# Performance work log

Hardware: AMD Instinct MI355X
Metric: run time of the kernel (lower is better)

The kernel has to match this reference:

```python
import jax, jax.numpy as jnp
import numpy as np

B, T, C, HS = 4, 2048, 1024, 16
H = C // HS
LAYER_ID, N_LAYER = 2, 24
D_MIX, D_DECAY = 32, 64
LN_EPS = 1e-5


def setup_inputs() -> dict:
    key = jax.random.key(0)
    ks = jax.random.split(key, 8)
    r01 = LAYER_ID / (N_LAYER - 1)
    r10 = 1.0 - LAYER_ID / N_LAYER
    ddd = (np.arange(C, dtype=np.float64) / C)
    tm = lambda p: (1.0 - ddd ** p).reshape(1, 1, C).astype(np.float32)
    time_maa_x = tm(r10)
    time_maa_w = tm(r10)
    time_maa_k = tm(r10)
    time_maa_v = (1.0 - (ddd ** r10 + 0.3 * r01)).reshape(1, 1, C).astype(np.float32)
    time_maa_r = tm(0.5 * r10)
    n = np.arange(C, dtype=np.float64)
    decay = (-6.0 + 5.0 * (n / (C - 1)) ** (0.7 + 1.3 * r01)).reshape(1, 1, C).astype(np.float32)
    zig = ((n + 1) % 3 - 1) * 0.1
    faaaa = (r01 * (1.0 - n / (C - 1)) + zig).reshape(H, HS).astype(np.float32)
    u01 = lambda k, s: jax.random.uniform(k, s, jnp.float32, -0.01, 0.01)
    return {
        "x": jax.random.normal(ks[0], (B, T, C), jnp.float32),
        "time_maa_x": jnp.asarray(time_maa_x),
        "time_maa_w": jnp.asarray(time_maa_w),
        "time_maa_k": jnp.asarray(time_maa_k),
        "time_maa_v": jnp.asarray(time_maa_v),
        "time_maa_r": jnp.asarray(time_maa_r),
        "time_maa_w1": u01(ks[1], (C, D_MIX * 4)),
        "time_maa_w2": u01(ks[2], (4, D_MIX, C)),
        "time_decay": jnp.asarray(decay),
        "time_decay_w1": u01(ks[3], (C, D_DECAY)),
        "time_decay_w2": u01(ks[4], (D_DECAY, C)),
        "time_faaaa": jnp.asarray(faaaa),
        "W_r": jax.random.normal(ks[5], (C, C), jnp.float32) * 0.02,
        "W_k": jax.random.normal(ks[6], (C, C), jnp.float32) * 0.02,
        "W_v": jax.random.normal(ks[7], (C, C), jnp.float32) * 0.02,
        "W_o": jax.random.normal(jax.random.fold_in(key, 99), (C, C), jnp.float32) * 0.02,
        "ln_g": jnp.ones((C,), jnp.float32),
        "ln_b": jnp.zeros((C,), jnp.float32),
    }


def _wkv6(r, k, v, w, u):
    # r,k,v,w: [B,T,H,N]; u: [H,N]. Per-head 16x16 state, rank-1 updates.
    wd = jnp.exp(-jnp.exp(w))  # decay in (0,1)
    rT, kT, vT, wT = (a.transpose(1, 0, 2, 3) for a in (r, k, v, wd))  # [T,B,H,N]

    def step(S, ins):
        r_t, k_t, v_t, w_t = ins  # each [B,H,N]
        kv = jnp.einsum("bhi,bhj->bhij", k_t, v_t)
        y_t = jnp.einsum("bhi,bhij->bhj", r_t, S + u[None, :, :, None] * kv)
        return w_t[..., None] * S + kv, y_t

    S0 = jnp.zeros((r.shape[0], H, HS, HS), r.dtype)
    _, ys = jax.lax.scan(step, S0, (rT, kT, vT, wT))  # ys: [T,B,H,N]
    return ys.transpose(1, 0, 2, 3)


def reference(x, time_maa_x, time_maa_w, time_maa_k, time_maa_v, time_maa_r,
              time_maa_w1, time_maa_w2, time_decay, time_decay_w1, time_decay_w2,
              time_faaaa, W_r, W_k, W_v, W_o, ln_g, ln_b):
    b, t, c = x.shape
    # time shift: previous token (zero at t=0)
    xx = jnp.concatenate([jnp.zeros_like(x[:, :1]), x[:, :-1]], axis=1) - x
    xxx = x + xx * time_maa_x
    m = jnp.tanh(xxx @ time_maa_w1).reshape(b, t, 4, D_MIX)
    m = jnp.einsum("btfd,fdc->fbtc", m, time_maa_w2)  # [4,B,T,C]
    mw, mk, mv, mr = m[0], m[1], m[2], m[3]
    xw = x + xx * (time_maa_w + mw)
    xk = x + xx * (time_maa_k + mk)
    xv = x + xx * (time_maa_v + mv)
    xr = x + xx * (time_maa_r + mr)
    r = (xr @ W_r).reshape(b, t, H, HS)
    k = (xk @ W_k).reshape(b, t, H, HS)
    v = (xv @ W_v).reshape(b, t, H, HS)
    ww = jnp.tanh(xw @ time_decay_w1) @ time_decay_w2
    w = (time_decay + ww).reshape(b, t, H, HS)
    y = _wkv6(r, k, v, w, time_faaaa).reshape(b, t, c)
    mu = jnp.mean(y, axis=-1, keepdims=True)
    var = jnp.mean(jnp.square(y - mu), axis=-1, keepdims=True)
    y = (y - mu) * jax.lax.rsqrt(var + LN_EPS) * ln_g + ln_b
    return y @ W_o
```

## Files before the change

### kernel.cpp

```cpp
#include <hip/hip_runtime.h>
#include <stdint.h>

#define TT 2048
#define CC 1024

typedef short bf16x8 __attribute__((ext_vector_type(8)));
typedef float f32x4 __attribute__((ext_vector_type(4)));
typedef unsigned uint2v __attribute__((ext_vector_type(2)));
typedef __attribute__((address_space(3))) uint32_t lds_u32_t;
typedef const __attribute__((address_space(1))) uint32_t glb_u32_t;

__device__ inline unsigned short f2b(float f) {
  union { float f; unsigned u; } c; c.f = f;
  unsigned u = c.u;
  return (unsigned short)((u + 0x7fffu + ((u >> 16) & 1u)) >> 16);
}
__device__ inline float b2f(unsigned short s) {
  union { unsigned u; float f; } c; c.u = ((unsigned)s) << 16; return c.f;
}

__device__ inline void gl_lds16(const void* g, void* l) {
  glb_u32_t* gp = (glb_u32_t*)(uintptr_t)g;
  lds_u32_t* lp = (lds_u32_t*)(uint32_t)(uintptr_t)l;
  __builtin_amdgcn_global_load_lds(gp, lp, 16, 0, 0);
}

__device__ inline void swiz(int& bx, int& by, int& bz) {
  int nx = gridDim.x, ny = gridDim.y;
  int flat = (blockIdx.z * ny + blockIdx.y) * nx + blockIdx.x;
  int xcd = flat & 7;
  int idx = flat >> 3;
  int perz = (nx * ny) >> 3;
  bz = idx / perz;
  int rem = idx - bz * perz;
  int r = rem / nx;
  bx = rem - r * nx;
  by = xcd * (ny >> 3) + r;
}

struct TSeg { const float* in; unsigned short* out; int R, C, tx, start; };
struct TransAll { TSeg seg[11]; int nseg; };
__global__ void transpose_all(TransAll ta) {
  __shared__ float tile[32][33];
  int bid = blockIdx.x;
  int si = 0;
  while (si + 1 < ta.nseg && bid >= ta.seg[si + 1].start) si++;
  TSeg sg = ta.seg[si];
  int lt = bid - sg.start;
  int bx = lt % sg.tx, by = lt / sg.tx;
  int c0 = bx * 32, r0 = by * 32;
  int tx = threadIdx.x, ty = threadIdx.y;
  for (int i = ty; i < 32; i += 8) {
    int r = r0 + i, c = c0 + tx;
    tile[i][tx] = (r < sg.R && c < sg.C) ? sg.in[(size_t)r * sg.C + c] : 0.f;
  }
  __syncthreads();
  int rr = r0 + tx;
  for (int i = ty; i < 32; i += 8) {
    int cc = c0 + i;
    if (cc < sg.C && rr < sg.R) sg.out[(size_t)cc * sg.R + rr] = f2b(tile[tx][i]);
  }
}

__global__ void shift_mix(const float* __restrict__ x, const float* __restrict__ tmx,
                          unsigned short* __restrict__ xb, unsigned short* __restrict__ xxb,
                          unsigned short* __restrict__ xxx) {
  int idx = blockIdx.x * 256 + threadIdx.x;
  int c4 = idx & 255;
  int row = idx >> 8;
  int t = row & (TT - 1);
  const float4* x4 = (const float4*)x;
  float4 xv = x4[idx];
  float4 pv = make_float4(0.f, 0.f, 0.f, 0.f);
  if (t > 0) pv = x4[idx - 256];
  float4 d;
  d.x = pv.x - xv.x; d.y = pv.y - xv.y; d.z = pv.z - xv.z; d.w = pv.w - xv.w;
  ushort4 ob;
  ob.x = f2b(xv.x); ob.y = f2b(xv.y); ob.z = f2b(xv.z); ob.w = f2b(xv.w);
  ((ushort4*)xb)[idx] = ob;
  ushort4 od;
  od.x = f2b(d.x); od.y = f2b(d.y); od.z = f2b(d.z); od.w = f2b(d.w);
  ((ushort4*)xxb)[idx] = od;
  float4 tm = ((const float4*)tmx)[c4];
  ushort4 o;
  o.x = f2b(xv.x + d.x * tm.x);
  o.y = f2b(xv.y + d.y * tm.y);
  o.z = f2b(xv.z + d.z * tm.z);
  o.w = f2b(xv.w + d.w * tm.w);
  ((ushort4*)xxx)[idx] = o;
}

__device__ __forceinline__ void gemm_core_pipe(
    const unsigned short* __restrict__ A, const unsigned short* __restrict__ Bt,
    int k0beg, int k0end, int lda, int ldb, int rowBase, int colBase,
    unsigned short* As, unsigned short* Bs, f32x4 acc[4][4], int w, int lane,
    int quad, int l16, int waveM, int waveN) {
#pragma unroll
  for (int i = 0; i < 4; i++)
#pragma unroll
    for (int j = 0; j < 4; j++) acc[i][j] = (f32x4){0.f, 0.f, 0.f, 0.f};
  const int SSB = 8192;
  const int nIter = (k0end - k0beg) >> 5;
  int rl = lane >> 2;
  int cl = (lane & 3) ^ ((lane >> 3) & 3);
  int rA0 = w * 16 + rl, rA1 = (w + 4) * 16 + rl;
  const unsigned short* gA0 = A + (size_t)(rowBase + rA0) * lda + cl * 8 + k0beg;
  const unsigned short* gA1 = A + (size_t)(rowBase + rA1) * lda + cl * 8 + k0beg;
  const unsigned short* gB0 = Bt + (size_t)(colBase + rA0) * ldb + cl * 8 + k0beg;
  const unsigned short* gB1 = Bt + (size_t)(colBase + rA1) * ldb + cl * 8 + k0beg;
  char* dA0 = (char*)As + w * 1024;
  char* dA1 = (char*)As + (w + 4) * 1024;
  char* dB0 = (char*)Bs + w * 1024;
  char* dB1 = (char*)Bs + (w + 4) * 1024;
  int sw = quad ^ ((l16 >> 1) & 3);
  int aoff = (waveM + l16) * 64 + sw * 16;
  int boff = (waveN + l16) * 64 + sw * 16;

#define ISSUE(it, st)                               \
  {                                                 \
    int ko = (it) * 32;                             \
    gl_lds16(gA0 + ko, dA0 + (st) * SSB);           \
    gl_lds16(gA1 + ko, dA1 + (st) * SSB);           \
    gl_lds16(gB0 + ko, dB0 + (st) * SSB);           \
    gl_lds16(gB1 + ko, dB1 + (st) * SSB);           \
  }

  ISSUE(0, 0)
  if (nIter > 1) ISSUE(1, 1)
  int stage = 0;
  for (int it = 0; it < nIter; ++it) {
    if (it + 1 < nIter) {
      asm volatile("s_waitcnt vmcnt(4)\ns_barrier" ::: "memory");
    } else {
      asm volatile("s_waitcnt vmcnt(0)\ns_barrier" ::: "memory");
    }
    if (it + 2 < nIter) {
      int ns = stage + 2; if (ns >= 3) ns -= 3;
      ISSUE(it + 2, ns)
    }
    const char* Ab = (const char*)As + stage * SSB;
    const char* Bb = (const char*)Bs + stage * SSB;
    bf16x8 af[4], bfr[4];
#pragma unroll
    for (int mt = 0; mt < 4; mt++)
      af[mt] = *(const bf16x8*)(Ab + aoff + mt * 1024);
#pragma unroll
    for (int nt = 0; nt < 4; nt++)
      bfr[nt] = *(const bf16x8*)(Bb + boff + nt * 1024);
#pragma unroll
    for (int mt = 0; mt < 4; mt++)
#pragma unroll
      for (int nt = 0; nt < 4; nt++)
        acc[mt][nt] = __builtin_amdgcn_mfma_f32_16x16x32_bf16(af[mt], bfr[nt], acc[mt][nt], 0, 0, 0);
    stage = stage + 1; if (stage >= 3) stage -= 3;
  }
#undef ISSUE
}

__global__ __launch_bounds__(256) void gemm_bf16(
    const unsigned short* __restrict__ A, const unsigned short* __restrict__ Bt,
    int N, int K, int lda, int ldb, int mode, int ldc,
    float* __restrict__ outF, unsigned short* __restrict__ outB,
    const float* __restrict__ tm) {
  __shared__ __align__(16) unsigned short As[3 * 4096];
  __shared__ __align__(16) unsigned short Bs[3 * 4096];
  int bx, by, bz;
  swiz(bx, by, bz);
  (void)bz;
  int tid = threadIdx.x;
  int w = tid >> 6, lane = tid & 63;
  int quad = lane >> 4, l16 = lane & 15;
  int rowBase = by * 128;
  int colBase = bx * 128;
  int waveM = (w >> 1) * 64, waveN = (w & 1) * 64;
  f32x4 acc[4][4];
  gemm_core_pipe(A, Bt, 0, K, lda, ldb, rowBase, colBase, As, Bs, acc, w, lane, quad, l16, waveM, waveN);
#pragma unroll
  for (int mt = 0; mt < 4; mt++)
#pragma unroll
    for (int nt = 0; nt < 4; nt++)
#pragma unroll
      for (int rg = 0; rg < 4; rg++) {
        int row = rowBase + waveM + mt * 16 + quad * 4 + rg;
        int col = colBase + waveN + nt * 16 + l16;
        if (col >= N) continue;
        float val = acc[mt][nt][rg];
        if (mode == 0) {
          outF[(size_t)row * ldc + col] = val;
        } else {
          int b = row >> 11, t = row & (TT - 1), h = col >> 4, n = col & 15;
          outF[(size_t)((b * 64 + h) * TT + t) * 16 + n] = expf(-expf(tm[col] + val));
        }
      }
}

__global__ __launch_bounds__(256) void gemm_splitk(
    const unsigned short* __restrict__ A, const unsigned short* __restrict__ Bt,
    int N, int Kc, int lda, int ldb, int ldp, float* __restrict__ part) {
  __shared__ __align__(16) unsigned short As[3 * 4096];
  __shared__ __align__(16) unsigned short Bs[3 * 4096];
  int s = blockIdx.x, by = blockIdx.y;
  int M = gridDim.y * 128;
  int tid = threadIdx.x;
  int w = tid >> 6, lane = tid & 63;
  int quad = lane >> 4, l16 = lane & 15;
  int rowBase = by * 128;
  int waveM = (w >> 1) * 64, waveN = (w & 1) * 64;
  f32x4 acc[4][4];
  gemm_core_pipe(A, Bt, s * Kc, (s + 1) * Kc, lda, ldb, rowBase, 0, As, Bs, acc, w, lane, quad, l16, waveM, waveN);
  float* pb = part + (size_t)s * M * ldp;
#pragma unroll
  for (int mt = 0; mt < 4; mt++)
#pragma unroll
    for (int nt = 0; nt < 4; nt++)
#pragma unroll
      for (int rg = 0; rg < 4; rg++) {
        int row = rowBase + waveM + mt * 16 + quad * 4 + rg;
        int col = waveN + nt * 16 + l16;
        if (col < N) pb[(size_t)row * ldp + col] = acc[mt][nt][rg];
      }
}

__global__ __launch_bounds__(256) void reduce_tanh(
    const float* __restrict__ part, unsigned short* __restrict__ out,
    int total4, int S, int strideElems) {
  int idx = blockIdx.x * 256 + threadIdx.x;
  if (idx >= total4) return;
  float4 a = ((const float4*)part)[idx];
  for (int s = 1; s < S; s++) {
    float4 b = ((const float4*)(part + (size_t)s * strideElems))[idx];
    a.x += b.x; a.y += b.y; a.z += b.z; a.w += b.w;
  }
  ushort4 o;
  o.x = f2b(tanhf(a.x)); o.y = f2b(tanhf(a.y));
  o.z = f2b(tanhf(a.z)); o.w = f2b(tanhf(a.w));
  ((ushort4*)out)[idx] = o;
}

struct GateArgs {
  const unsigned short* A;
  const unsigned short* Bt;
  unsigned short* out[4];
  const float* tm[4];
  const unsigned short* xb;
  const unsigned short* xxb;
};
__global__ __launch_bounds__(256) void gemm_gate4(GateArgs ga) {
  __shared__ __align__(16) unsigned short As[3 * 4096];
  __shared__ __align__(16) unsigned short Bs[3 * 4096];
  int flat = (blockIdx.z * 64 + blockIdx.y) * 8 + blockIdx.x;
  int xcd = flat & 7;
  int idx = flat >> 3;
  int z = idx & 3;
  int tile = idx >> 2;
  int by = xcd * 8 + (tile >> 3);
  int bx = tile & 7;
  const unsigned short* A = ga.A + z * 32;
  const unsigned short* Bt = ga.Bt + (size_t)z * 1024 * 32;
  unsigned short* outB = ga.out[z];
  const float* tm = ga.tm[z];
  int tid = threadIdx.x;
  int w = tid >> 6, lane = tid & 63;
  int quad = lane >> 4, l16 = lane & 15;
  int rowBase = by * 128;
  int colBase = bx * 128;
  int waveM = (w >> 1) * 64, waveN = (w & 1) * 64;
  f32x4 acc[4][4];
  gemm_core_pipe(A, Bt, 0, 32, 128, 32, rowBase, colBase, As, Bs, acc, w, lane, quad, l16, waveM, waveN);
#pragma unroll
  for (int mt = 0; mt < 4; mt++)
#pragma unroll
    for (int nt = 0; nt < 4; nt++)
#pragma unroll
      for (int rg = 0; rg < 4; rg++) {
        int row = rowBase + waveM + mt * 16 + quad * 4 + rg;
        int col = colBase + waveN + nt * 16 + l16;
        size_t o = (size_t)row * CC + col;
        float xv = b2f(ga.xb[o]), xxv = b2f(ga.xxb[o]);
        outB[o] = f2b(xv + xxv * (tm[col] + acc[mt][nt][rg]));
      }
}

struct ProjArgs {
  const unsigned short* A[3];
  const unsigned short* Bt[3];
  unsigned short* out[3];
};
__global__ __launch_bounds__(256) void gemm_proj3(ProjArgs pa) {
  __shared__ __align__(16) unsigned short As[3 * 4096];
  __shared__ __align__(16) unsigned short Bs[3 * 4096];
  int bx, by, bz;
  swiz(bx, by, bz);
  const unsigned short* A = pa.A[bz];
  const unsigned short* Bt = pa.Bt[bz];
  unsigned short* outB = pa.out[bz];
  int tid = threadIdx.x;
  int w = tid >> 6, lane = tid & 63;
  int quad = lane >> 4, l16 = lane & 15;
  int rowBase = by * 128;
  int colBase = bx * 128;
  int waveM = (w >> 1) * 64, waveN = (w & 1) * 64;
  f32x4 acc[4][4];
  gemm_core_pipe(A, Bt, 0, 1024, 1024, 1024, rowBase, colBase, As, Bs, acc, w, lane, quad, l16, waveM, waveN);
#pragma unroll
  for (int mt = 0; mt < 4; mt++)
#pragma unroll
    for (int nt = 0; nt < 4; nt++)
#pragma unroll
      for (int rg = 0; rg < 4; rg++) {
        int row = rowBase + waveM + mt * 16 + quad * 4 + rg;
        int col = colBase + waveN + nt * 16 + l16;
        int b = row >> 11, t = row & (TT - 1), h = col >> 4, n = col & 15;
        outB[(size_t)((b * 64 + h) * TT + t) * 16 + n] = f2b(acc[mt][nt][rg]);
      }
}

__device__ __forceinline__ float reduce_p(float part) {
#if __has_builtin(__builtin_amdgcn_permlane32_swap) && __has_builtin(__builtin_amdgcn_permlane16_swap)
  uint2v a = __builtin_amdgcn_permlane32_swap(__float_as_uint(part), __float_as_uint(part), false, false);
  float s1 = part + __uint_as_float(a.y);
  uint2v b = __builtin_amdgcn_permlane16_swap(__float_as_uint(s1), __float_as_uint(s1), false, false);
  return s1 + __uint_as_float(b.y);
#else
  part += __shfl_xor(part, 16, 64);
  part += __shfl_xor(part, 32, 64);
  return part;
#endif
}

__global__ __launch_bounds__(1024) void wkv_scan2(
    const unsigned short* __restrict__ r, const unsigned short* __restrict__ k,
    const unsigned short* __restrict__ v, const float* __restrict__ wd,
    const float* __restrict__ u, float* __restrict__ y) {
  __shared__ __align__(16) unsigned short lrb[16][256];
  __shared__ __align__(16) unsigned short lkb[16][256];
  __shared__ __align__(16) unsigned short lvb[16][256];
  __shared__ __align__(16) float lw[16][256];
  __shared__ __align__(16) float Lend[16][256];
  __shared__ __align__(16) float Sini[16][256];
  __shared__ float Eend[16][16];
  int bh = blockIdx.x;
  int b = bh >> 6, h = bh & 63;
  int tid = threadIdx.x;
  int c = tid >> 6, lane = tid & 63;
  int j = lane & 15, p = lane >> 4;
  size_t base = (size_t)bh * TT * 16 + (size_t)c * 128 * 16;

  float S0 = 0.f, S1 = 0.f, S2 = 0.f, S3 = 0.f;
  float E0 = 1.f, E1 = 1.f, E2 = 1.f, E3 = 1.f;
  for (int t0 = 0; t0 < 128; t0 += 16) {
    size_t off = base + (size_t)t0 * 16;
    ushort4 kv4 = ((const ushort4*)(k + off))[lane];
    ushort4 vv = ((const ushort4*)(v + off))[lane];
    float4 wv = ((const float4*)(wd + off))[lane];
    ((ushort4*)lkb[c])[lane] = kv4;
    ((ushort4*)lvb[c])[lane] = vv;
    ((float4*)lw[c])[lane] = wv;
#pragma unroll
    for (int s = 0; s < 16; s++) {
      ushort4 kk = *(const ushort4*)(lkb[c] + s * 16 + p * 4);
      float4 ww = *(const float4*)(lw[c] + s * 16 + p * 4);
      float vj = b2f(lvb[c][s * 16 + j]);
      S0 = fmaf(ww.x, S0, b2f(kk.x) * vj); E0 *= ww.x;
      S1 = fmaf(ww.y, S1, b2f(kk.y) * vj); E1 *= ww.y;
      S2 = fmaf(ww.z, S2, b2f(kk.z) * vj); E2 *= ww.z;
      S3 = fmaf(ww.w, S3, b2f(kk.w) * vj); E3 *= ww.w;
    }
  }
  Lend[c][(p * 4 + 0) * 16 + j] = S0;
  Lend[c][(p * 4 + 1) * 16 + j] = S1;
  Lend[c][(p * 4 + 2) * 16 + j] = S2;
  Lend[c][(p * 4 + 3) * 16 + j] = S3;
  if (j == 0) {
    Eend[c][p * 4 + 0] = E0;
    Eend[c][p * 4 + 1] = E1;
    Eend[c][p * 4 + 2] = E2;
    Eend[c][p * 4 + 3] = E3;
  }
  __syncthreads();

  if (c == 0) {
    float T0 = 0.f, T1 = 0.f, T2 = 0.f, T3 = 0.f;
    for (int cc = 0; cc < 16; cc++) {
      Sini[cc][(p * 4 + 0) * 16 + j] = T0;
      Sini[cc][(p * 4 + 1) * 16 + j] = T1;
      Sini[cc][(p * 4 + 2) * 16 + j] = T2;
      Sini[cc][(p * 4 + 3) * 16 + j] = T3;
      float e0 = Eend[cc][p * 4 + 0], e1 = Eend[cc][p * 4 + 1];
      float e2 = Eend[cc][p * 4 + 2], e3 = Eend[cc][p * 4 + 3];
      T0 = fmaf(e0, T0, Lend[cc][(p * 4 + 0) * 16 + j]);
      T1 = fmaf(e1, T1, Lend[cc][(p * 4 + 1) * 16 + j]);
      T2 = fmaf(e2, T2, Lend[cc][(p * 4 + 2) * 16 + j]);
      T3 = fmaf(e3, T3, Lend[cc][(p * 4 + 3) * 16 + j]);
    }
  }
  __syncthreads();

  float u0 = u[h * 16 + p * 4 + 0], u1 = u[h * 16 + p * 4 + 1];
  float u2 = u[h * 16 + p * 4 + 2], u3 = u[h * 16 + p * 4 + 3];
  S0 = Sini[c][(p * 4 + 0) * 16 + j];
  S1 = Sini[c][(p * 4 + 1) * 16 + j];
  S2 = Sini[c][(p * 4 + 2) * 16 + j];
  S3 = Sini[c][(p * 4 + 3) * 16 + j];
  for (int t0 = 0; t0 < 128; t0 += 16) {
    size_t off = base + (size_t)t0 * 16;
    ushort4 rv = ((const ushort4*)(r + off))[lane];
    ushort4 kv4 = ((const ushort4*)(k + off))[lane];
    ushort4 vv = ((const ushort4*)(v + off))[lane];
    float4 wv = ((const float4*)(wd + off))[lane];
    ((ushort4*)lrb[c])[lane] = rv;
    ((ushort4*)lkb[c])[lane] = kv4;
    ((ushort4*)lvb[c])[lane] = vv;
    ((float4*)lw[c])[lane] = wv;
#pragma unroll
    for (int s = 0; s < 16; s++) {
      ushort4 rr4 = *(const ushort4*)(lrb[c] + s * 16 + p * 4);
      ushort4 kk4 = *(const ushort4*)(lkb[c] + s * 16 + p * 4);
      float4 ww = *(const float4*)(lw[c] + s * 16 + p * 4);
      float vj = b2f(lvb[c][s * 16 + j]);
      float kv, part;
      kv = b2f(kk4.x) * vj; part = b2f(rr4.x) * fmaf(u0, kv, S0); S0 = fmaf(ww.x, S0, kv);
      kv = b2f(kk4.y) * vj; part = fmaf(b2f(rr4.y), fmaf(u1, kv, S1), part); S1 = fmaf(ww.y, S1, kv);
      kv = b2f(kk4.z) * vj; part = fmaf(b2f(rr4.z), fmaf(u2, kv, S2), part); S2 = fmaf(ww.z, S2, kv);
      kv = b2f(kk4.w) * vj; part = fmaf(b2f(rr4.w), fmaf(u3, kv, S3), part); S3 = fmaf(ww.w, S3, kv);
      float tot = reduce_p(part);
      if (p == 0) y[(size_t)(b * TT + c * 128 + t0 + s) * CC + h * 16 + j] = tot;
    }
  }
}

__global__ __launch_bounds__(256) void ln_fused(const float* __restrict__ y,
                                                const float* __restrict__ g,
                                                const float* __restrict__ be,
                                                unsigned short* __restrict__ out) {
  int row = blockIdx.x;
  int tid = threadIdx.x;
  float4 val = ((const float4*)(y + (size_t)row * CC))[tid];
  float s = val.x + val.y + val.z + val.w;
  float sq = val.x * val.x + val.y * val.y + val.z * val.z + val.w * val.w;
#pragma unroll
  for (int m = 1; m < 64; m <<= 1) {
    s += __shfl_xor(s, m, 64);
    sq += __shfl_xor(sq, m, 64);
  }
  __shared__ float ss[4], s2[4];
  int w = tid >> 6;
  if ((tid & 63) == 0) { ss[w] = s; s2[w] = sq; }
  __syncthreads();
  s = ss[0] + ss[1] + ss[2] + ss[3];
  sq = s2[0] + s2[1] + s2[2] + s2[3];
  float mu = s * (1.f / 1024.f);
  float var = sq * (1.f / 1024.f) - mu * mu;
  float rstd = rsqrtf(var + 1e-5f);
  float4 gg = ((const float4*)g)[tid];
  float4 bb = ((const float4*)be)[tid];
  ushort4 o;
  o.x = f2b((val.x - mu) * rstd * gg.x + bb.x);
  o.y = f2b((val.y - mu) * rstd * gg.y + bb.y);
  o.z = f2b((val.z - mu) * rstd * gg.z + bb.z);
  o.w = f2b((val.w - mu) * rstd * gg.w + bb.w);
  ((ushort4*)(out + (size_t)row * CC))[tid] = o;
}

extern "C" void kernel_launch(void* const* d_in, const int* in_sizes, int n_in,
                              void* d_out, int out_size, void* d_ws, size_t ws_size,
                              hipStream_t stream) {
  (void)in_sizes; (void)n_in; (void)out_size; (void)ws_size;
  const float* x = (const float*)d_in[0];
  const float* tmx = (const float*)d_in[1];
  const float* tmw = (const float*)d_in[2];
  const float* tmk = (const float*)d_in[3];
  const float* tmv = (const float*)d_in[4];
  const float* tmr = (const float*)d_in[5];
  const float* w1 = (const float*)d_in[6];
  const float* w2 = (const float*)d_in[7];
  const float* tdecay = (const float*)d_in[8];
  const float* dw1 = (const float*)d_in[9];
  const float* dw2 = (const float*)d_in[10];
  const float* faaaa = (const float*)d_in[11];
  const float* Wr = (const float*)d_in[12];
  const float* Wk = (const float*)d_in[13];
  const float* Wv = (const float*)d_in[14];
  const float* Wo = (const float*)d_in[15];
  const float* lng = (const float*)d_in[16];
  const float* lnb = (const float*)d_in[17];
  float* out = (float*)d_out;

  char* ws = (char*)d_ws;
  const size_t MBy = 1ull << 20;
  unsigned short* rb   = (unsigned short*)(ws + 0);
  unsigned short* kbuf = (unsigned short*)(ws + 16 * MBy);
  unsigned short* vbuf = (unsigned short*)(ws + 32 * MBy);
  float* wdb = (float*)(ws + 48 * MBy);
  unsigned short* xb    = (unsigned short*)(ws + 80 * MBy);
  unsigned short* xxb16 = (unsigned short*)(ws + 96 * MBy);
  float* yb = (float*)(ws + 80 * MBy);
  unsigned short* xxxb = (unsigned short*)(ws + 112 * MBy);
  unsigned short* xwb  = (unsigned short*)(ws + 112 * MBy);
  unsigned short* xrb  = (unsigned short*)(ws + 128 * MBy);
  unsigned short* xkb  = (unsigned short*)(ws + 144 * MBy);
  unsigned short* ynb  = (unsigned short*)(ws + 144 * MBy);
  unsigned short* xvb  = (unsigned short*)(ws + 160 * MBy);
  float* mixP  = (float*)(ws + 128 * MBy);
  float* decP  = (float*)(ws + 0);
  unsigned short* mtmpb = (unsigned short*)(ws + 176 * MBy);
  unsigned short* dtmpb = (unsigned short*)(ws + 178 * MBy);
  char* wreg = ws + 179 * MBy;
  unsigned short* w1t  = (unsigned short*)(wreg);
  unsigned short* w2t  = (unsigned short*)(wreg + 256 * 1024);
  unsigned short* dw1t = (unsigned short*)(wreg + 512 * 1024);
  unsigned short* dw2t = (unsigned short*)(wreg + 768 * 1024);
  unsigned short* Wrt  = (unsigned short*)(wreg + 1024 * 1024);
  unsigned short* Wkt = Wrt + 1024 * 1024;
  unsigned short* Wvt = Wkt + 1024 * 1024;
  unsigned short* Wot = Wvt + 1024 * 1024;

  dim3 tb(32, 8);
  {
    TransAll ta;
    int st = 0, si = 0;
    auto add = [&](const float* in, unsigned short* o, int R, int C) {
      int tx = (C + 31) / 32, ty = (R + 31) / 32;
      ta.seg[si++] = TSeg{in, o, R, C, tx, st};
      st += tx * ty;
    };
    add(Wr, Wrt, 1024, 1024);
    add(Wk, Wkt, 1024, 1024);
    add(Wv, Wvt, 1024, 1024);
    add(Wo, Wot, 1024, 1024);
    for (int g = 0; g < 4; g++)
      add(w2 + (size_t)g * 32 * 1024, w2t + (size_t)g * 1024 * 32, 32, 1024);
    add(w1, w1t, 1024, 128);
    add(dw1, dw1t, 1024, 64);
    add(dw2, dw2t, 64, 1024);
    ta.nseg = si;
    transpose_all<<<st, tb, 0, stream>>>(ta);
  }

  shift_mix<<<8192, 256, 0, stream>>>(x, tmx, xb, xxb16, xxxb);

  gemm_splitk<<<dim3(4, 64), 256, 0, stream>>>(xxxb, w1t, 128, 256, 1024, 1024, 128, mixP);
  reduce_tanh<<<1024, 256, 0, stream>>>(mixP, mtmpb, 8192 * 128 / 4, 4, 8192 * 128);

  {
    GateArgs ga;
    ga.A = mtmpb; ga.Bt = w2t;
    ga.out[0] = xwb; ga.out[1] = xkb; ga.out[2] = xvb; ga.out[3] = xrb;
    ga.tm[0] = tmw; ga.tm[1] = tmk; ga.tm[2] = tmv; ga.tm[3] = tmr;
    ga.xb = xb; ga.xxb = xxb16;
    gemm_gate4<<<dim3(8, 64, 4), 256, 0, stream>>>(ga);
  }
  gemm_splitk<<<dim3(4, 64), 256, 0, stream>>>(xwb, dw1t, 64, 256, 1024, 1024, 64, decP);
  reduce_tanh<<<512, 256, 0, stream>>>(decP, dtmpb, 8192 * 64 / 4, 4, 8192 * 64);
  gemm_bf16<<<dim3(8, 64), 256, 0, stream>>>(dtmpb, dw2t, 1024, 64, 64, 64, 4, 1024,
                                             wdb, nullptr, tdecay);
  {
    ProjArgs pa;
    pa.A[0] = xrb; pa.A[1] = xkb; pa.A[2] = xvb;
    pa.Bt[0] = Wrt; pa.Bt[1] = Wkt; pa.Bt[2] = Wvt;
    pa.out[0] = rb; pa.out[1] = kbuf; pa.out[2] = vbuf;
    gemm_proj3<<<dim3(8, 64, 3), 256, 0, stream>>>(pa);
  }

  wkv_scan2<<<256, 1024, 0, stream>>>(rb, kbuf, vbuf, wdb, faaaa, yb);
  ln_fused<<<8192, 256, 0, stream>>>(yb, lng, lnb, ynb);
  gemm_bf16<<<dim3(8, 64), 256, 0, stream>>>(ynb, Wot, 1024, 1024, 1024, 1024, 0, 1024,
                                             out, nullptr, nullptr);
}
```

Measured before the change: 381.5 us.

## Enlarge GEMM tiles to 256x128 for projection and output GEMMs

```diff
diff --git a/kernel.cpp b/kernel.cpp
--- a/kernel.cpp
+++ b/kernel.cpp
@@ -157,12 +157,94 @@
 #undef ISSUE
 }
 
-__global__ __launch_bounds__(256) void gemm_bf16(
+__device__ __forceinline__ void gemm_core_pipe256(
+    const unsigned short* __restrict__ A, const unsigned short* __restrict__ Bt,
+    int k0beg, int k0end, int lda, int ldb, int rowBase, int colBase,
+    unsigned short* As, unsigned short* Bs, f32x4 acc[8][4], int w, int lane,
+    int quad, int l16, int waveM, int waveN) {
+#pragma unroll
+  for (int i = 0; i < 8; i++)
+#pragma unroll
+    for (int j = 0; j < 4; j++) acc[i][j] = (f32x4){0.f, 0.f, 0.f, 0.f};
+  const int SSA = 16384;
+  const int SSB = 8192;
+  const int nIter = (k0end - k0beg) >> 5;
+  int rl = lane >> 2;
+  int cl = (lane & 3) ^ ((lane >> 3) & 3);
+  const unsigned short* gA[4];
+  char* dA[4];
+#pragma unroll
+  for (int i = 0; i < 4; i++) {
+    int g = w + 4 * i;
+    gA[i] = A + (size_t)(rowBase + g * 16 + rl) * lda + cl * 8 + k0beg;
+    dA[i] = (char*)As + g * 1024;
+  }
+  const unsigned short* gB[2];
+  char* dB[2];
+#pragma unroll
+  for (int i = 0; i < 2; i++) {
+    int g = w + 4 * i;
+    gB[i] = Bt + (size_t)(colBase + g * 16 + rl) * ldb + cl * 8 + k0beg;
+    dB[i] = (char*)Bs + g * 1024;
+  }
+  int sw = quad ^ ((l16 >> 1) & 3);
+  int aoff = (waveM + l16) * 64 + sw * 16;
+  int boff = (waveN + l16) * 64 + sw * 16;
+
+#define ISSUE2(it, st)                                  \
+  {                                                     \
+    int ko = (it) * 32;                                 \
+    gl_lds16(gA[0] + ko, dA[0] + (st) * SSA);           \
+    gl_lds16(gA[1] + ko, dA[1] + (st) * SSA);           \
+    gl_lds16(gA[2] + ko, dA[2] + (st) * SSA);           \
+    gl_lds16(gA[3] + ko, dA[3] + (st) * SSA);           \
+    gl_lds16(gB[0] + ko, dB[0] + (st) * SSB);           \
+    gl_lds16(gB[1] + ko, dB[1] + (st) * SSB);           \
+  }
+
+  ISSUE2(0, 0)
+  if (nIter > 1) ISSUE2(1, 1)
+  int stage = 0;
+  for (int it = 0; it < nIter; ++it) {
+    if (it + 1 < nIter) {
+      asm volatile("s_waitcnt vmcnt(6)\ns_barrier" ::: "memory");
+    } else {
+      asm volatile("s_waitcnt vmcnt(0)\ns_barrier" ::: "memory");
+    }
+    if (it + 2 < nIter) {
+      int ns = stage + 2; if (ns >= 3) ns -= 3;
+      ISSUE2(it + 2, ns)
+    }
+    const char* Ab = (const char*)As + stage * SSA;
+    const char* Bb = (const char*)Bs + stage * SSB;
+    bf16x8 bfr[4];
+#pragma unroll
+    for (int nt = 0; nt < 4; nt++)
+      bfr[nt] = *(const bf16x8*)(Bb + boff + nt * 1024);
+#pragma unroll
+    for (int mh = 0; mh < 2; mh++) {
+      bf16x8 af[4];
+#pragma unroll
+      for (int i = 0; i < 4; i++)
+        af[i] = *(const bf16x8*)(Ab + aoff + (mh * 4 + i) * 1024);
+#pragma unroll
+      for (int i = 0; i < 4; i++)
+#pragma unroll
+        for (int nt = 0; nt < 4; nt++)
+          acc[mh * 4 + i][nt] =
+              __builtin_amdgcn_mfma_f32_16x16x32_bf16(af[i], bfr[nt], acc[mh * 4 + i][nt], 0, 0, 0);
+    }
+    stage = stage + 1; if (stage >= 3) stage -= 3;
+  }
+#undef ISSUE2
+}
+
+__global__ __launch_bounds__(256, 2) void gemm_bf16(
     const unsigned short* __restrict__ A, const unsigned short* __restrict__ Bt,
     int N, int K, int lda, int ldb, int mode, int ldc,
     float* __restrict__ outF, unsigned short* __restrict__ outB,
     const float* __restrict__ tm) {
-  __shared__ __align__(16) unsigned short As[3 * 4096];
+  __shared__ __align__(16) unsigned short As[3 * 8192];
   __shared__ __align__(16) unsigned short Bs[3 * 4096];
   int bx, by, bz;
   swiz(bx, by, bz);
@@ -170,13 +252,13 @@
   int tid = threadIdx.x;
   int w = tid >> 6, lane = tid & 63;
   int quad = lane >> 4, l16 = lane & 15;
-  int rowBase = by * 128;
+  int rowBase = by * 256;
   int colBase = bx * 128;
-  int waveM = (w >> 1) * 64, waveN = (w & 1) * 64;
-  f32x4 acc[4][4];
-  gemm_core_pipe(A, Bt, 0, K, lda, ldb, rowBase, colBase, As, Bs, acc, w, lane, quad, l16, waveM, waveN);
-#pragma unroll
-  for (int mt = 0; mt < 4; mt++)
+  int waveM = (w >> 1) * 128, waveN = (w & 1) * 64;
+  f32x4 acc[8][4];
+  gemm_core_pipe256(A, Bt, 0, K, lda, ldb, rowBase, colBase, As, Bs, acc, w, lane, quad, l16, waveM, waveN);
+#pragma unroll
+  for (int mt = 0; mt < 8; mt++)
 #pragma unroll
     for (int nt = 0; nt < 4; nt++)
 #pragma unroll
@@ -286,8 +368,8 @@
   const unsigned short* Bt[3];
   unsigned short* out[3];
 };
-__global__ __launch_bounds__(256) void gemm_proj3(ProjArgs pa) {
-  __shared__ __align__(16) unsigned short As[3 * 4096];
+__global__ __launch_bounds__(256, 2) void gemm_proj3(ProjArgs pa) {
+  __shared__ __align__(16) unsigned short As[3 * 8192];
   __shared__ __align__(16) unsigned short Bs[3 * 4096];
   int bx, by, bz;
   swiz(bx, by, bz);
@@ -297,13 +379,13 @@
   int tid = threadIdx.x;
   int w = tid >> 6, lane = tid & 63;
   int quad = lane >> 4, l16 = lane & 15;
-  int rowBase = by * 128;
+  int rowBase = by * 256;
   int colBase = bx * 128;
-  int waveM = (w >> 1) * 64, waveN = (w & 1) * 64;
-  f32x4 acc[4][4];
-  gemm_core_pipe(A, Bt, 0, 1024, 1024, 1024, rowBase, colBase, As, Bs, acc, w, lane, quad, l16, waveM, waveN);
-#pragma unroll
-  for (int mt = 0; mt < 4; mt++)
+  int waveM = (w >> 1) * 128, waveN = (w & 1) * 64;
+  f32x4 acc[8][4];
+  gemm_core_pipe256(A, Bt, 0, 1024, 1024, 1024, rowBase, colBase, As, Bs, acc, w, lane, quad, l16, waveM, waveN);
+#pragma unroll
+  for (int mt = 0; mt < 8; mt++)
 #pragma unroll
     for (int nt = 0; nt < 4; nt++)
 #pragma unroll
@@ -552,18 +634,18 @@
   }
   gemm_splitk<<<dim3(4, 64), 256, 0, stream>>>(xwb, dw1t, 64, 256, 1024, 1024, 64, decP);
   reduce_tanh<<<512, 256, 0, stream>>>(decP, dtmpb, 8192 * 64 / 4, 4, 8192 * 64);
-  gemm_bf16<<<dim3(8, 64), 256, 0, stream>>>(dtmpb, dw2t, 1024, 64, 64, 64, 4, 1024,
+  gemm_bf16<<<dim3(8, 32), 256, 0, stream>>>(dtmpb, dw2t, 1024, 64, 64, 64, 4, 1024,
                                              wdb, nullptr, tdecay);
   {
     ProjArgs pa;
     pa.A[0] = xrb; pa.A[1] = xkb; pa.A[2] = xvb;
     pa.Bt[0] = Wrt; pa.Bt[1] = Wkt; pa.Bt[2] = Wvt;
     pa.out[0] = rb; pa.out[1] = kbuf; pa.out[2] = vbuf;
-    gemm_proj3<<<dim3(8, 64, 3), 256, 0, stream>>>(pa);
+    gemm_proj3<<<dim3(8, 32, 3), 256, 0, stream>>>(pa);
   }
 
   wkv_scan2<<<256, 1024, 0, stream>>>(rb, kbuf, vbuf, wdb, faaaa, yb);
   ln_fused<<<8192, 256, 0, stream>>>(yb, lng, lnb, ynb);
-  gemm_bf16<<<dim3(8, 64), 256, 0, stream>>>(ynb, Wot, 1024, 1024, 1024, 1024, 0, 1024,
+  gemm_bf16<<<dim3(8, 32), 256, 0, stream>>>(ynb, Wot, 1024, 1024, 1024, 1024, 0, 1024,
                                              out, nullptr, nullptr);
 }
```

Measured after the change: 446.2 us. +17.0%, slower.

## Rewrite projection GEMM with 256x256 tiles, 8 waves and 4-stage pipeline

Applied to the files above, without the earlier changes.

```diff
diff --git a/kernel.cpp b/kernel.cpp
--- a/kernel.cpp
+++ b/kernel.cpp
@@ -286,9 +286,9 @@
   const unsigned short* Bt[3];
   unsigned short* out[3];
 };
-__global__ __launch_bounds__(256) void gemm_proj3(ProjArgs pa) {
-  __shared__ __align__(16) unsigned short As[3 * 4096];
-  __shared__ __align__(16) unsigned short Bs[3 * 4096];
+__global__ __launch_bounds__(512, 2) void gemm_proj3_8ph(ProjArgs pa) {
+  __shared__ __align__(16) unsigned short As[4 * 8192];
+  __shared__ __align__(16) unsigned short Bs[4 * 8192];
   int bx, by, bz;
   swiz(bx, by, bz);
   const unsigned short* A = pa.A[bz];
@@ -297,21 +297,95 @@
   int tid = threadIdx.x;
   int w = tid >> 6, lane = tid & 63;
   int quad = lane >> 4, l16 = lane & 15;
-  int rowBase = by * 128;
-  int colBase = bx * 128;
-  int waveM = (w >> 1) * 64, waveN = (w & 1) * 64;
-  f32x4 acc[4][4];
-  gemm_core_pipe(A, Bt, 0, 1024, 1024, 1024, rowBase, colBase, As, Bs, acc, w, lane, quad, l16, waveM, waveN);
-#pragma unroll
-  for (int mt = 0; mt < 4; mt++)
+  int wr = w >> 2, wc = w & 3;
+  int rowBase = by * 256, colBase = bx * 256;
+  int rl = lane >> 2;
+  int cl = (lane & 3) ^ ((lane >> 3) & 3);
+  const unsigned short* gA0 = A + (size_t)(rowBase + w * 16 + rl) * 1024 + cl * 8;
+  const unsigned short* gA1 = A + (size_t)(rowBase + (w + 8) * 16 + rl) * 1024 + cl * 8;
+  const unsigned short* gB0 = Bt + (size_t)(colBase + w * 16 + rl) * 1024 + cl * 8;
+  const unsigned short* gB1 = Bt + (size_t)(colBase + (w + 8) * 16 + rl) * 1024 + cl * 8;
+  char* dA0 = (char*)As + w * 1024;
+  char* dA1 = (char*)As + (w + 8) * 1024;
+  char* dB0 = (char*)Bs + w * 1024;
+  char* dB1 = (char*)Bs + (w + 8) * 1024;
+  int sw = quad ^ ((l16 >> 1) & 3);
+  int aoffB = wr * 8192 + l16 * 64 + sw * 16;
+  int boffB = wc * 4096 + l16 * 64 + sw * 16;
+  f32x4 acc[8][4];
+#pragma unroll
+  for (int i = 0; i < 8; i++)
+#pragma unroll
+    for (int j = 0; j < 4; j++) acc[i][j] = (f32x4){0.f, 0.f, 0.f, 0.f};
+
+#define STG_A(h)                                          \
+  { int kc = (h) * 32, sl = ((h) & 3) * 16384;            \
+    gl_lds16(gA0 + kc, dA0 + sl);                         \
+    gl_lds16(gA1 + kc, dA1 + sl); }
+#define STG_B(h)                                          \
+  { int kc = (h) * 32, sl = ((h) & 3) * 16384;            \
+    gl_lds16(gB0 + kc, dB0 + sl);                         \
+    gl_lds16(gB1 + kc, dB1 + sl); }
+
+  STG_A(0) STG_B(0) STG_A(1) STG_B(1) STG_A(2) STG_B(2)
+  asm volatile("s_waitcnt vmcnt(8)" ::: "memory");
+  __builtin_amdgcn_s_barrier();
+
+  for (int h = 0; h < 32; ++h) {
+    const char* Ab = (const char*)As + (h & 3) * 16384;
+    const char* Bb = (const char*)Bs + (h & 3) * 16384;
+    bf16x8 bfr[4], af[4];
 #pragma unroll
     for (int nt = 0; nt < 4; nt++)
+      bfr[nt] = *(const bf16x8*)(Bb + boffB + nt * 1024);
+#pragma unroll
+    for (int i = 0; i < 4; i++)
+      af[i] = *(const bf16x8*)(Ab + aoffB + i * 1024);
+    if (h + 3 < 32) STG_A(h + 3)
+    __builtin_amdgcn_s_barrier();
+    __builtin_amdgcn_s_setprio(1);
+#pragma unroll
+    for (int i = 0; i < 4; i++)
+#pragma unroll
+      for (int nt = 0; nt < 4; nt++)
+        acc[i][nt] = __builtin_amdgcn_mfma_f32_16x16x32_bf16(af[i], bfr[nt], acc[i][nt], 0, 0, 0);
+    __builtin_amdgcn_s_setprio(0);
+    __builtin_amdgcn_s_barrier();
+    bf16x8 ag[4];
+#pragma unroll
+    for (int i = 0; i < 4; i++)
+      ag[i] = *(const bf16x8*)(Ab + aoffB + (4 + i) * 1024);
+    if (h + 3 < 32) STG_B(h + 3)
+    __builtin_amdgcn_s_barrier();
+    __builtin_amdgcn_s_setprio(1);
+#pragma unroll
+    for (int i = 0; i < 4; i++)
+#pragma unroll
+      for (int nt = 0; nt < 4; nt++)
+        acc[4 + i][nt] = __builtin_amdgcn_mfma_f32_16x16x32_bf16(ag[i], bfr[nt], acc[4 + i][nt], 0, 0, 0);
+    __builtin_amdgcn_s_setprio(0);
+    if (h < 29) {
+      asm volatile("s_waitcnt vmcnt(8)" ::: "memory");
+    } else if (h == 29) {
+      asm volatile("s_waitcnt vmcnt(4)" ::: "memory");
+    } else {
+      asm volatile("s_waitcnt vmcnt(0)" ::: "memory");
+    }
+    __builtin_amdgcn_s_barrier();
+  }
+#undef STG_A
+#undef STG_B
+
+#pragma unroll
+  for (int mt = 0; mt < 8; mt++)
+#pragma unroll
+    for (int nt = 0; nt < 4; nt++)
 #pragma unroll
       for (int rg = 0; rg < 4; rg++) {
-        int row = rowBase + waveM + mt * 16 + quad * 4 + rg;
-        int col = colBase + waveN + nt * 16 + l16;
-        int b = row >> 11, t = row & (TT - 1), h = col >> 4, n = col & 15;
-        outB[(size_t)((b * 64 + h) * TT + t) * 16 + n] = f2b(acc[mt][nt][rg]);
+        int row = rowBase + wr * 128 + mt * 16 + quad * 4 + rg;
+        int col = colBase + wc * 64 + nt * 16 + l16;
+        int b = row >> 11, t = row & (TT - 1), hh = col >> 4, n = col & 15;
+        outB[(size_t)((b * 64 + hh) * TT + t) * 16 + n] = f2b(acc[mt][nt][rg]);
       }
 }
 
@@ -559,7 +633,7 @@
     pa.A[0] = xrb; pa.A[1] = xkb; pa.A[2] = xvb;
     pa.Bt[0] = Wrt; pa.Bt[1] = Wkt; pa.Bt[2] = Wvt;
     pa.out[0] = rb; pa.out[1] = kbuf; pa.out[2] = vbuf;
-    gemm_proj3<<<dim3(8, 64, 3), 256, 0, stream>>>(pa);
+    gemm_proj3_8ph<<<dim3(4, 32, 3), 512, 0, stream>>>(pa);
   }
 
   wkv_scan2<<<256, 1024, 0, stream>>>(rb, kbuf, vbuf, wdb, faaaa, yb);
```

Result: no change. 378.3 us (-0.8%).

## Rewrite RKV projection GEMM with 256x128 tiles, 8 waves, 4-stage LDS pipeline

Applied to the files above, without the earlier changes.

```diff
diff --git a/kernel.cpp b/kernel.cpp
--- a/kernel.cpp
+++ b/kernel.cpp
@@ -286,9 +286,9 @@
   const unsigned short* Bt[3];
   unsigned short* out[3];
 };
-__global__ __launch_bounds__(256) void gemm_proj3(ProjArgs pa) {
-  __shared__ __align__(16) unsigned short As[3 * 4096];
-  __shared__ __align__(16) unsigned short Bs[3 * 4096];
+__global__ __launch_bounds__(512, 2) void gemm_proj3_8ph(ProjArgs pa) {
+  __shared__ __align__(16) unsigned short As[4 * 8192];
+  __shared__ __align__(16) unsigned short Bs[4 * 4096];
   int bx, by, bz;
   swiz(bx, by, bz);
   const unsigned short* A = pa.A[bz];
@@ -297,21 +297,73 @@
   int tid = threadIdx.x;
   int w = tid >> 6, lane = tid & 63;
   int quad = lane >> 4, l16 = lane & 15;
-  int rowBase = by * 128;
-  int colBase = bx * 128;
-  int waveM = (w >> 1) * 64, waveN = (w & 1) * 64;
+  int wr = w >> 1, wc = w & 1;
+  int rowBase = by * 256, colBase = bx * 128;
+  int rl = lane >> 2;
+  int cl = (lane & 3) ^ ((lane >> 3) & 3);
+  const unsigned short* gA0 = A + (size_t)(rowBase + w * 16 + rl) * 1024 + cl * 8;
+  const unsigned short* gA1 = A + (size_t)(rowBase + (w + 8) * 16 + rl) * 1024 + cl * 8;
+  const unsigned short* gB0 = Bt + (size_t)(colBase + w * 16 + rl) * 1024 + cl * 8;
+  char* dA0 = (char*)As + w * 1024;
+  char* dA1 = (char*)As + (w + 8) * 1024;
+  char* dB0 = (char*)Bs + w * 1024;
+  int sw = quad ^ ((l16 >> 1) & 3);
+  int aoffB = wr * 4096 + l16 * 64 + sw * 16;
+  int boffB = wc * 4096 + l16 * 64 + sw * 16;
   f32x4 acc[4][4];
-  gemm_core_pipe(A, Bt, 0, 1024, 1024, 1024, rowBase, colBase, As, Bs, acc, w, lane, quad, l16, waveM, waveN);
+#pragma unroll
+  for (int i = 0; i < 4; i++)
+#pragma unroll
+    for (int j = 0; j < 4; j++) acc[i][j] = (f32x4){0.f, 0.f, 0.f, 0.f};
+
+#define STG(h)                                            \
+  { int kc = (h) * 32;                                    \
+    int slA = ((h) & 3) * 16384, slB = ((h) & 3) * 8192;  \
+    gl_lds16(gA0 + kc, dA0 + slA);                        \
+    gl_lds16(gA1 + kc, dA1 + slA);                        \
+    gl_lds16(gB0 + kc, dB0 + slB); }
+
+  STG(0) STG(1) STG(2)
+  asm volatile("s_waitcnt vmcnt(6)\ns_barrier" ::: "memory");
+
+  for (int h = 0; h < 32; ++h) {
+    const char* Ab = (const char*)As + (h & 3) * 16384;
+    const char* Bb = (const char*)Bs + (h & 3) * 8192;
+    bf16x8 af[4], bfr[4];
+#pragma unroll
+    for (int nt = 0; nt < 4; nt++)
+      bfr[nt] = *(const bf16x8*)(Bb + boffB + nt * 1024);
+#pragma unroll
+    for (int mt = 0; mt < 4; mt++)
+      af[mt] = *(const bf16x8*)(Ab + aoffB + mt * 1024);
+    if (h + 3 < 32) STG(h + 3)
+    __builtin_amdgcn_s_setprio(1);
+#pragma unroll
+    for (int mt = 0; mt < 4; mt++)
+#pragma unroll
+      for (int nt = 0; nt < 4; nt++)
+        acc[mt][nt] = __builtin_amdgcn_mfma_f32_16x16x32_bf16(af[mt], bfr[nt], acc[mt][nt], 0, 0, 0);
+    __builtin_amdgcn_s_setprio(0);
+    if (h <= 28) {
+      asm volatile("s_waitcnt vmcnt(6) lgkmcnt(0)\ns_barrier" ::: "memory");
+    } else if (h == 29) {
+      asm volatile("s_waitcnt vmcnt(3) lgkmcnt(0)\ns_barrier" ::: "memory");
+    } else if (h == 30) {
+      asm volatile("s_waitcnt vmcnt(0) lgkmcnt(0)\ns_barrier" ::: "memory");
+    }
+  }
+#undef STG
+
 #pragma unroll
   for (int mt = 0; mt < 4; mt++)
 #pragma unroll
     for (int nt = 0; nt < 4; nt++)
 #pragma unroll
       for (int rg = 0; rg < 4; rg++) {
-        int row = rowBase + waveM + mt * 16 + quad * 4 + rg;
-        int col = colBase + waveN + nt * 16 + l16;
-        int b = row >> 11, t = row & (TT - 1), h = col >> 4, n = col & 15;
-        outB[(size_t)((b * 64 + h) * TT + t) * 16 + n] = f2b(acc[mt][nt][rg]);
+        int row = rowBase + wr * 64 + mt * 16 + quad * 4 + rg;
+        int col = colBase + wc * 64 + nt * 16 + l16;
+        int b = row >> 11, t = row & (TT - 1), hh = col >> 4, n = col & 15;
+        outB[(size_t)((b * 64 + hh) * TT + t) * 16 + n] = f2b(acc[mt][nt][rg]);
       }
 }
 
@@ -559,7 +611,7 @@
     pa.A[0] = xrb; pa.A[1] = xkb; pa.A[2] = xvb;
     pa.Bt[0] = Wrt; pa.Bt[1] = Wkt; pa.Bt[2] = Wvt;
     pa.out[0] = rb; pa.out[1] = kbuf; pa.out[2] = vbuf;
-    gemm_proj3<<<dim3(8, 64, 3), 256, 0, stream>>>(pa);
+    gemm_proj3_8ph<<<dim3(8, 32, 3), 512, 0, stream>>>(pa);
   }
 
   wkv_scan2<<<256, 1024, 0, stream>>>(rb, kbuf, vbuf, wdb, faaaa, yb);
```

After: 371.6 us. 1.03x faster.
